# Optimization experiments

Measured on AMD Instinct MI355X. Metric: run time of the kernel, lower is better.

Reference implementation:

```python
import jax, jax.numpy as jnp
import numpy as np

N_SRC = 50000
N_DST = 50000
E = 800000
IN_DIM = 128
OUT_DIM = 64
HEADS = 4
NEG_SLOPE = 0.2  # PyG GATConv default negative_slope
EPS = 1e-16      # PyG softmax denominator epsilon


def setup_inputs() -> dict:
    key = jax.random.key(0)
    ks = jax.random.split(key, 8)
    x_src = jax.random.normal(ks[0], (N_SRC, IN_DIM), dtype=jnp.float32)
    x_dst = jax.random.normal(ks[1], (N_DST, IN_DIM), dtype=jnp.float32)
    src = jax.random.randint(ks[2], (E,), 0, N_SRC, dtype=jnp.int32)
    dst = jax.random.randint(ks[3], (E,), 0, N_DST, dtype=jnp.int32)
    edge_index = jnp.stack([src, dst], axis=0)
    W_src = jax.random.normal(ks[4], (IN_DIM, HEADS * OUT_DIM), dtype=jnp.float32) / np.sqrt(IN_DIM)
    W_dst = jax.random.normal(ks[5], (IN_DIM, HEADS * OUT_DIM), dtype=jnp.float32) / np.sqrt(IN_DIM)
    att_src = jax.random.normal(ks[6], (HEADS, OUT_DIM), dtype=jnp.float32) / np.sqrt(OUT_DIM)
    att_dst = jax.random.normal(ks[7], (HEADS, OUT_DIM), dtype=jnp.float32) / np.sqrt(OUT_DIM)
    bias = jnp.zeros((OUT_DIM,), dtype=jnp.float32)
    return {"x_src": x_src, "x_dst": x_dst, "edge_index": edge_index,
            "W_src": W_src, "W_dst": W_dst, "att_src": att_src,
            "att_dst": att_dst, "bias": bias}


def reference(x_src, x_dst, edge_index, W_src, W_dst, att_src, att_dst, bias):
    # Linear projections -> [N, H, C]
    hs = (x_src @ W_src).reshape(N_SRC, HEADS, OUT_DIM)
    hd = (x_dst @ W_dst).reshape(N_DST, HEADS, OUT_DIM)
    # Per-node attention logits -> [N, H]
    a_s = jnp.einsum('nhc,hc->nh', hs, att_src)
    a_d = jnp.einsum('nhc,hc->nh', hd, att_dst)

    src, dst = edge_index[0], edge_index[1]
    # Per-edge logits [E, H]
    alpha = jax.nn.leaky_relu(a_s[src] + a_d[dst], negative_slope=NEG_SLOPE)
    # Segment softmax over edges sharing the same dst node
    amax = jax.ops.segment_max(alpha, dst, num_segments=N_DST)
    alpha = jnp.exp(alpha - amax[dst])
    denom = jax.ops.segment_sum(alpha, dst, num_segments=N_DST)
    alpha = alpha / (denom[dst] + EPS)
    # (dropout=0 / eval mode: no attention dropout)
    # Message + scatter-add aggregation: out[i] = sum_e alpha_e * hs[src_e]
    msg = hs[src] * alpha[:, :, None]                 # [E, H, C]
    out = jax.ops.segment_sum(msg, dst, num_segments=N_DST)  # [N_dst, H, C]
    # concat=False -> mean over heads, then bias
    return out.mean(axis=1) + bias
```

## Files before the change

kernel.cpp:

```cpp
#include <hip/hip_runtime.h>
#include <hip/hip_bf16.h>

#define N_SRC 50000
#define N_DST 50000
#define NEDGE 800000
#define IND   128
#define HEADS 4
#define CDIM  64
#define HC    256
#define MAXDEG 96
#define NB_ALPHA 12500
#define NB_HIST  3125

typedef _Float16 half8  __attribute__((ext_vector_type(8)));
typedef _Float16 half2t __attribute__((ext_vector_type(2)));
typedef float    f32x4  __attribute__((ext_vector_type(4)));

static __device__ __forceinline__ unsigned int pack2h(float a, float b) {
    union { half2t h; unsigned int u; } v;
    v.h[0] = (_Float16)a; v.h[1] = (_Float16)b;
    return v.u;
}
static __device__ __forceinline__ half2t bits2h(unsigned int u) {
    union { unsigned int u; half2t h; } v; v.u = u; return v.h;
}

__global__ void prep_kernel(const float* __restrict__ Wdst,
                            const float* __restrict__ att_d,
                            float* __restrict__ WdA,
                            const float* __restrict__ Wsrc,
                            _Float16* __restrict__ WhT, int* __restrict__ deg) {
    int b = blockIdx.x, tid = threadIdx.x;
    if (b < 196) {
        int i = b * 256 + tid;
        if (i < N_DST) deg[i] = 0;
    } else if (b < 198) {
        int id = (b - 196) * 256 + tid;
        int k = id >> 2, h = id & 3;
        float acc = 0.f;
        for (int c = 0; c < CDIM; ++c)
            acc += Wdst[k * HC + h * CDIM + c] * att_d[h * CDIM + c];
        WdA[id] = acc;
    } else {
        int idx = (b - 198) * 256 + tid;
        int n = idx >> 7, k = idx & 127;
        WhT[idx] = (_Float16)Wsrc[k * HC + n];
    }
}

__global__ __launch_bounds__(256) void gemm_mfma_kernel(
        const float* __restrict__ x, const _Float16* __restrict__ WhT,
        const float* __restrict__ att_s,
        unsigned short* __restrict__ hsTh, float* __restrict__ a_s) {
    int tid = threadIdx.x;
    int w = tid >> 6, lane = tid & 63;
    int ll = lane & 15, q = lane >> 4;
    int rbase = blockIdx.x * 64 + w * 16;

    int arow = rbase + ll;
    if (arow >= N_SRC) arow = N_SRC - 1;
    const float* xr = x + (size_t)arow * IND + q * 8;
    half8 afrag[4];
    #pragma unroll
    for (int kf = 0; kf < 4; ++kf) {
        float4 u0 = *(const float4*)(xr + kf * 32);
        float4 u1 = *(const float4*)(xr + kf * 32 + 4);
        half8 a;
        a[0] = (_Float16)u0.x; a[1] = (_Float16)u0.y;
        a[2] = (_Float16)u0.z; a[3] = (_Float16)u0.w;
        a[4] = (_Float16)u1.x; a[5] = (_Float16)u1.y;
        a[6] = (_Float16)u1.z; a[7] = (_Float16)u1.w;
        afrag[kf] = a;
    }

    f32x4 acc[16];
    #pragma unroll
    for (int t = 0; t < 16; ++t) acc[t] = (f32x4){0.f, 0.f, 0.f, 0.f};

    #pragma unroll
    for (int t = 0; t < 16; ++t) {
        const _Float16* bp = WhT + (size_t)(t * 16 + ll) * IND + q * 8;
        half8 b0 = *(const half8*)(bp + 0);
        half8 b1 = *(const half8*)(bp + 32);
        half8 b2 = *(const half8*)(bp + 64);
        half8 b3 = *(const half8*)(bp + 96);
        f32x4 c = acc[t];
        c = __builtin_amdgcn_mfma_f32_16x16x32_f16(afrag[0], b0, c, 0, 0, 0);
        c = __builtin_amdgcn_mfma_f32_16x16x32_f16(afrag[1], b1, c, 0, 0, 0);
        c = __builtin_amdgcn_mfma_f32_16x16x32_f16(afrag[2], b2, c, 0, 0, 0);
        c = __builtin_amdgcn_mfma_f32_16x16x32_f16(afrag[3], b3, c, 0, 0, 0);
        acc[t] = c;
    }

    #pragma unroll
    for (int tg = 0; tg < 4; ++tg) {
        #pragma unroll
        for (int r = 0; r < 4; ++r) {
            int n = rbase + q * 4 + r;
            if (n < N_SRC) {
                uint2 v;
                v.x = pack2h(acc[tg     ][r], acc[tg + 4 ][r]);
                v.y = pack2h(acc[tg + 8 ][r], acc[tg + 12][r]);
                *(uint2*)(hsTh + (size_t)n * HC + (tg * 16 + ll) * 4) = v;
            }
        }
    }

    float attv[16];
    #pragma unroll
    for (int t = 0; t < 16; ++t) attv[t] = att_s[t * 16 + ll];
    #pragma unroll
    for (int r = 0; r < 4; ++r) {
        float4 p;
        p.x = acc[0][r]*attv[0]  + acc[1][r]*attv[1]  + acc[2][r]*attv[2]  + acc[3][r]*attv[3];
        p.y = acc[4][r]*attv[4]  + acc[5][r]*attv[5]  + acc[6][r]*attv[6]  + acc[7][r]*attv[7];
        p.z = acc[8][r]*attv[8]  + acc[9][r]*attv[9]  + acc[10][r]*attv[10]+ acc[11][r]*attv[11];
        p.w = acc[12][r]*attv[12]+ acc[13][r]*attv[13]+ acc[14][r]*attv[14]+ acc[15][r]*attv[15];
        #pragma unroll
        for (int off = 1; off < 16; off <<= 1) {
            p.x += __shfl_xor(p.x, off, 64);
            p.y += __shfl_xor(p.y, off, 64);
            p.z += __shfl_xor(p.z, off, 64);
            p.w += __shfl_xor(p.w, off, 64);
        }
        int n = rbase + q * 4 + r;
        if (ll == 0 && n < N_SRC) *(float4*)(a_s + (size_t)n * 4) = p;
    }
}

__global__ __launch_bounds__(256) void mid_kernel(
        const float* __restrict__ x_dst, const float* __restrict__ WdA,
        float* __restrict__ a_d,
        const int* __restrict__ src, const int* __restrict__ dst,
        int* __restrict__ deg, int* __restrict__ col2) {
    int b = blockIdx.x, tid = threadIdx.x;
    if (b < NB_ALPHA) {
        int n    = (b * 256 + tid) >> 6;
        int lane = tid & 63;
        const float* xp = x_dst + (size_t)n * IND;
        const float4* wa = (const float4*)WdA;
        float x0 = xp[lane], x1 = xp[lane + 64];
        float4 wa0 = wa[lane], wa1 = wa[lane + 64];
        float p0 = x0 * wa0.x + x1 * wa1.x;
        float p1 = x0 * wa0.y + x1 * wa1.y;
        float p2 = x0 * wa0.z + x1 * wa1.z;
        float p3 = x0 * wa0.w + x1 * wa1.w;
        for (int off = 32; off >= 1; off >>= 1) {
            p0 += __shfl_xor(p0, off, 64);
            p1 += __shfl_xor(p1, off, 64);
            p2 += __shfl_xor(p2, off, 64);
            p3 += __shfl_xor(p3, off, 64);
        }
        if (lane == 0) {
            a_d[n * 4 + 0] = p0; a_d[n * 4 + 1] = p1;
            a_d[n * 4 + 2] = p2; a_d[n * 4 + 3] = p3;
        }
    } else {
        int e = (b - NB_ALPHA) * 256 + tid;
        if (e < NEDGE) {
            int d = dst[e];
            int r = atomicAdd(&deg[d], 1);
            if (r < MAXDEG) col2[d * MAXDEG + r] = src[e];
        }
    }
}

__global__ __launch_bounds__(256) void aggregate_kernel(
        const int* __restrict__ deg, const int* __restrict__ col2,
        const float4* __restrict__ as4, const float4* __restrict__ ad4,
        const unsigned short* __restrict__ hsTh,
        const float* __restrict__ bias, float* __restrict__ out) {
    __shared__ int   s_off[4][MAXDEG];
    __shared__ uint4 s_pk[4][MAXDEG];
    int tid = threadIdx.x;
    int wv = tid >> 6, lane = tid & 63;
    int i = (blockIdx.x * 256 + tid) >> 6;
    if (i >= N_DST) return;
    int dg = deg[i]; if (dg > MAXDEG) dg = MAXDEG;
    float bv = bias[lane];
    if (dg == 0) { out[i * CDIM + lane] = bv; return; }
    float4 ad = ad4[i];
    const int* crow = col2 + i * MAXDEG;

    float s0 = 0.f, s1 = 0.f, s2 = 0.f, s3 = 0.f;
    for (int e = lane; e < dg; e += 64) {
        int sn = crow[e];
        float4 av = as4[sn];
        float lx = av.x + ad.x; lx = lx > 0.f ? lx : 0.2f * lx;
        float ly = av.y + ad.y; ly = ly > 0.f ? ly : 0.2f * ly;
        float lz = av.z + ad.z; lz = lz > 0.f ? lz : 0.2f * lz;
        float lw = av.w + ad.w; lw = lw > 0.f ? lw : 0.2f * lw;
        float w0 = __expf(lx), w1 = __expf(ly), w2 = __expf(lz), w3 = __expf(lw);
        s0 += w0; s1 += w1; s2 += w2; s3 += w3;
        s_off[wv][e] = sn * HC;
        float4 wf = {w0, w1, w2, w3};
        *(float4*)&s_pk[wv][e] = wf;
    }
    for (int off = 32; off >= 1; off >>= 1) {
        s0 += __shfl_xor(s0, off, 64);
        s1 += __shfl_xor(s1, off, 64);
        s2 += __shfl_xor(s2, off, 64);
        s3 += __shfl_xor(s3, off, 64);
    }
    float i0 = 0.25f / (s0 + 1e-16f);
    float i1 = 0.25f / (s1 + 1e-16f);
    float i2 = 0.25f / (s2 + 1e-16f);
    float i3 = 0.25f / (s3 + 1e-16f);

    for (int e = lane; e < dg; e += 64) {
        float4 wf = *(float4*)&s_pk[wv][e];
        uint4 pk;
        pk.x = (unsigned int)s_off[wv][e];
        pk.y = pack2h(wf.x * i0, wf.y * i1);
        pk.z = pack2h(wf.z * i2, wf.w * i3);
        pk.w = 0;
        s_pk[wv][e] = pk;
    }
    __asm__ volatile("s_waitcnt lgkmcnt(0)" ::: "memory");

    const unsigned short* hb = hsTh + (lane << 2);
    float acc = 0.f;
    int j = 0;
    for (; j + 4 <= dg; j += 4) {
        uint4 p0 = s_pk[wv][j];
        uint4 p1 = s_pk[wv][j + 1];
        uint4 p2 = s_pk[wv][j + 2];
        uint4 p3 = s_pk[wv][j + 3];
        uint2 h0 = *(const uint2*)(hb + p0.x);
        uint2 h1 = *(const uint2*)(hb + p1.x);
        uint2 h2 = *(const uint2*)(hb + p2.x);
        uint2 h3 = *(const uint2*)(hb + p3.x);
        acc = __builtin_amdgcn_fdot2(bits2h(h0.x), bits2h(p0.y), acc, false);
        acc = __builtin_amdgcn_fdot2(bits2h(h0.y), bits2h(p0.z), acc, false);
        acc = __builtin_amdgcn_fdot2(bits2h(h1.x), bits2h(p1.y), acc, false);
        acc = __builtin_amdgcn_fdot2(bits2h(h1.y), bits2h(p1.z), acc, false);
        acc = __builtin_amdgcn_fdot2(bits2h(h2.x), bits2h(p2.y), acc, false);
        acc = __builtin_amdgcn_fdot2(bits2h(h2.y), bits2h(p2.z), acc, false);
        acc = __builtin_amdgcn_fdot2(bits2h(h3.x), bits2h(p3.y), acc, false);
        acc = __builtin_amdgcn_fdot2(bits2h(h3.y), bits2h(p3.z), acc, false);
    }
    for (; j < dg; ++j) {
        uint4 p0 = s_pk[wv][j];
        uint2 h0 = *(const uint2*)(hb + p0.x);
        acc = __builtin_amdgcn_fdot2(bits2h(h0.x), bits2h(p0.y), acc, false);
        acc = __builtin_amdgcn_fdot2(bits2h(h0.y), bits2h(p0.z), acc, false);
    }
    out[i * CDIM + lane] = acc + bv;
}

extern "C" void kernel_launch(void* const* d_in, const int* in_sizes, int n_in,
                              void* d_out, int out_size, void* d_ws, size_t ws_size,
                              hipStream_t stream) {
    const float* x_src   = (const float*)d_in[0];
    const float* x_dst   = (const float*)d_in[1];
    const int*   ei      = (const int*)d_in[2];
    const float* W_src   = (const float*)d_in[3];
    const float* W_dst   = (const float*)d_in[4];
    const float* att_src = (const float*)d_in[5];
    const float* att_dst = (const float*)d_in[6];
    const float* bias    = (const float*)d_in[7];
    float* out = (float*)d_out;

    char* ws = (char*)d_ws;
    unsigned short* hsTh = (unsigned short*)ws; ws += (size_t)N_SRC * HC * 2;
    int*    col2    = (int*)ws;    ws += (size_t)N_DST * MAXDEG * 4;
    float*  a_s     = (float*)ws;  ws += (size_t)N_SRC * 4 * 4;
    float*  a_d     = (float*)ws;  ws += (size_t)N_DST * 4 * 4;
    float*  WdA     = (float*)ws;  ws += 2048;
    _Float16* WhT   = (_Float16*)ws; ws += IND * HC * 2;
    int*    deg     = (int*)ws;    ws += N_DST * 4;

    prep_kernel<<<326, 256, 0, stream>>>(W_dst, att_dst, WdA, W_src, WhT, deg);
    gemm_mfma_kernel<<<(N_SRC + 63) / 64, 256, 0, stream>>>(x_src, WhT, att_src, hsTh, a_s);
    mid_kernel<<<NB_ALPHA + NB_HIST, 256, 0, stream>>>(x_dst, WdA, a_d, ei, ei + NEDGE, deg, col2);
    aggregate_kernel<<<(N_DST + 3) / 4, 256, 0, stream>>>(deg, col2,
                                                          (const float4*)a_s, (const float4*)a_d,
                                                          hsTh, bias, out);
}
```

Before: 256.7 us.

## Partition CSR histogram build by destination range across block groups

Restructures the edge bucketing pass so that 8 groups of blocks each read all edges with vectorized nontemporal loads but only handle destinations in their own range of 6250 nodes. The aim is to localize atomics and col2 writes into a smaller address window per group, which likely maps to distinct XCDs and L2 slices, and to issue the histogram blocks before the a_d projection blocks. The cost is that every edge is read 8 times and most lanes do filtered no-op work.

New measurement: 243.6 us. 1.05x faster.

```diff
diff --git a/kernel.cpp b/kernel.cpp
--- a/kernel.cpp
+++ b/kernel.cpp
@@ -10,11 +10,14 @@
 #define HC    256
 #define MAXDEG 96
 #define NB_ALPHA 12500
-#define NB_HIST  3125
+#define HIST_GPB 256
+#define NB_HIST2 2048
+#define DPG 6250
 
 typedef _Float16 half8  __attribute__((ext_vector_type(8)));
 typedef _Float16 half2t __attribute__((ext_vector_type(2)));
 typedef float    f32x4  __attribute__((ext_vector_type(4)));
+typedef int      i32x4  __attribute__((ext_vector_type(4)));
 
 static __device__ __forceinline__ unsigned int pack2h(float a, float b) {
     union { half2t h; unsigned int u; } v;
@@ -134,8 +137,28 @@
         const int* __restrict__ src, const int* __restrict__ dst,
         int* __restrict__ deg, int* __restrict__ col2) {
     int b = blockIdx.x, tid = threadIdx.x;
-    if (b < NB_ALPHA) {
-        int n    = (b * 256 + tid) >> 6;
+    if (b < NB_HIST2) {
+        int g  = b & 7;
+        int bg = b >> 3;
+        int lo = g * DPG, hi = lo + DPG;
+        #pragma unroll 1
+        for (int it = 0; it < 4; ++it) {
+            int base = ((it * HIST_GPB + bg) << 10) + (tid << 2);
+            if (base >= NEDGE) break;
+            i32x4 dv = __builtin_nontemporal_load((const i32x4*)(dst + base));
+            i32x4 sv = __builtin_nontemporal_load((const i32x4*)(src + base));
+            #pragma unroll
+            for (int j = 0; j < 4; ++j) {
+                int d = dv[j];
+                if (d >= lo && d < hi) {
+                    int r = atomicAdd(&deg[d], 1);
+                    if (r < MAXDEG) col2[d * MAXDEG + r] = sv[j];
+                }
+            }
+        }
+    } else {
+        int rank = b - NB_HIST2;
+        int n    = (rank * 256 + tid) >> 6;
         int lane = tid & 63;
         const float* xp = x_dst + (size_t)n * IND;
         const float4* wa = (const float4*)WdA;
@@ -154,13 +177,6 @@
         if (lane == 0) {
             a_d[n * 4 + 0] = p0; a_d[n * 4 + 1] = p1;
             a_d[n * 4 + 2] = p2; a_d[n * 4 + 3] = p3;
-        }
-    } else {
-        int e = (b - NB_ALPHA) * 256 + tid;
-        if (e < NEDGE) {
-            int d = dst[e];
-            int r = atomicAdd(&deg[d], 1);
-            if (r < MAXDEG) col2[d * MAXDEG + r] = src[e];
         }
     }
 }
@@ -272,7 +288,7 @@
 
     prep_kernel<<<326, 256, 0, stream>>>(W_dst, att_dst, WdA, W_src, WhT, deg);
     gemm_mfma_kernel<<<(N_SRC + 63) / 64, 256, 0, stream>>>(x_src, WhT, att_src, hsTh, a_s);
-    mid_kernel<<<NB_ALPHA + NB_HIST, 256, 0, stream>>>(x_dst, WdA, a_d, ei, ei + NEDGE, deg, col2);
+    mid_kernel<<<NB_HIST2 + NB_ALPHA, 256, 0, stream>>>(x_dst, WdA, a_d, ei, ei + NEDGE, deg, col2);
     aggregate_kernel<<<(N_DST + 3) / 4, 256, 0, stream>>>(deg, col2,
                                                           (const float4*)a_s, (const float4*)a_d,
                                                           hsTh, bias, out);
```

## Two-pass bucketed CSR build: bin edges by destination range before scattering

Applied to the files above, without the earlier changes.

Edge insertion into the per-destination adjacency lists is split into two kernels. The first bins edges into 64 queues keyed by destination group and block parity, using wave-aggregated atomics, and packs the local destination and source into one word. The second kernel has the blocks of each destination group scatter only within that group's 6250 destinations, so the deg atomics and col2 writes stay within a smaller, more cache-resident address window. This costs an extra pass over the edges, an extra launch and queue storage. It also relies on the source id fitting in 17 bits and on no queue exceeding QCAP.

New measurement: 993.2 us. 3.87x slower.

```diff
diff --git a/kernel.cpp b/kernel.cpp
--- a/kernel.cpp
+++ b/kernel.cpp
@@ -9,8 +9,12 @@
 #define CDIM  64
 #define HC    256
 #define MAXDEG 96
-#define NB_ALPHA 12500
-#define NB_HIST  3125
+#define NB_ALPHA  12500
+#define NB_BUCKET 3125
+#define NB_SCAT   2048
+#define DPG  6250
+#define QCAP 16384
+#define NQ   64
 
 typedef _Float16 half8  __attribute__((ext_vector_type(8)));
 typedef _Float16 half2t __attribute__((ext_vector_type(2)));
@@ -29,11 +33,13 @@
                             const float* __restrict__ att_d,
                             float* __restrict__ WdA,
                             const float* __restrict__ Wsrc,
-                            _Float16* __restrict__ WhT, int* __restrict__ deg) {
+                            _Float16* __restrict__ WhT, int* __restrict__ deg,
+                            int* __restrict__ qtail) {
     int b = blockIdx.x, tid = threadIdx.x;
     if (b < 196) {
         int i = b * 256 + tid;
         if (i < N_DST) deg[i] = 0;
+        if (b == 0 && tid < NQ) qtail[tid] = 0;
     } else if (b < 198) {
         int id = (b - 196) * 256 + tid;
         int k = id >> 2, h = id & 3;
@@ -128,14 +134,37 @@
     }
 }
 
-__global__ __launch_bounds__(256) void mid_kernel(
+__global__ __launch_bounds__(256) void mid1_kernel(
         const float* __restrict__ x_dst, const float* __restrict__ WdA,
         float* __restrict__ a_d,
         const int* __restrict__ src, const int* __restrict__ dst,
-        int* __restrict__ deg, int* __restrict__ col2) {
+        unsigned int* __restrict__ q, int* __restrict__ qtail) {
     int b = blockIdx.x, tid = threadIdx.x;
-    if (b < NB_ALPHA) {
-        int n    = (b * 256 + tid) >> 6;
+    if (b < NB_BUCKET) {
+        int e = b * 256 + tid;
+        int d = __builtin_nontemporal_load(dst + e);
+        int s = __builtin_nontemporal_load(src + e);
+        unsigned int g    = (unsigned int)d / DPG;
+        unsigned int dloc = (unsigned int)d - g * DPG;
+        unsigned int v    = (dloc << 17) | (unsigned int)s;
+        int lane = tid & 63;
+        int qi = (int)g * 8 + (b & 7);
+        #pragma unroll
+        for (unsigned int gi = 0; gi < 8; ++gi) {
+            unsigned long long m = __ballot(g == gi);
+            if (g == gi) {
+                int leader = __ffsll(m) - 1;
+                int myoff  = __popcll(m & ((1ull << lane) - 1ull));
+                int base = 0;
+                if (lane == leader) base = atomicAdd(&qtail[qi], __popcll(m));
+                base = __shfl(base, leader, 64);
+                int slot = base + myoff;
+                if (slot < QCAP) q[(size_t)qi * QCAP + slot] = v;
+            }
+        }
+    } else {
+        int rank = b - NB_BUCKET;
+        int n    = (rank * 256 + tid) >> 6;
         int lane = tid & 63;
         const float* xp = x_dst + (size_t)n * IND;
         const float4* wa = (const float4*)WdA;
@@ -155,12 +184,27 @@
             a_d[n * 4 + 0] = p0; a_d[n * 4 + 1] = p1;
             a_d[n * 4 + 2] = p2; a_d[n * 4 + 3] = p3;
         }
-    } else {
-        int e = (b - NB_ALPHA) * 256 + tid;
-        if (e < NEDGE) {
-            int d = dst[e];
+    }
+}
+
+__global__ __launch_bounds__(256) void mid2_kernel(
+        const unsigned int* __restrict__ q, const int* __restrict__ qtail,
+        int* __restrict__ deg, int* __restrict__ col2) {
+    int b = blockIdx.x, tid = threadIdx.x;
+    int g  = b & 7;
+    int bg = b >> 3;
+    int base_d = g * DPG;
+    #pragma unroll 1
+    for (int sq = 0; sq < 8; ++sq) {
+        int qi = g * 8 + sq;
+        int n = qtail[qi]; if (n > QCAP) n = QCAP;
+        const unsigned int* qp = q + (size_t)qi * QCAP;
+        for (int idx = bg * 256 + tid; idx < n; idx += NB_SCAT / 8 * 256) {
+            unsigned int v = qp[idx];
+            int s = (int)(v & 0x1FFFFu);
+            int d = base_d + (int)(v >> 17);
             int r = atomicAdd(&deg[d], 1);
-            if (r < MAXDEG) col2[d * MAXDEG + r] = src[e];
+            if (r < MAXDEG) col2[d * MAXDEG + r] = s;
         }
     }
 }
@@ -264,15 +308,19 @@
     char* ws = (char*)d_ws;
     unsigned short* hsTh = (unsigned short*)ws; ws += (size_t)N_SRC * HC * 2;
     int*    col2    = (int*)ws;    ws += (size_t)N_DST * MAXDEG * 4;
+    unsigned int* q = (unsigned int*)ws; ws += (size_t)NQ * QCAP * 4;
     float*  a_s     = (float*)ws;  ws += (size_t)N_SRC * 4 * 4;
     float*  a_d     = (float*)ws;  ws += (size_t)N_DST * 4 * 4;
     float*  WdA     = (float*)ws;  ws += 2048;
     _Float16* WhT   = (_Float16*)ws; ws += IND * HC * 2;
     int*    deg     = (int*)ws;    ws += N_DST * 4;
-
-    prep_kernel<<<326, 256, 0, stream>>>(W_dst, att_dst, WdA, W_src, WhT, deg);
+    int*    qtail   = (int*)ws;    ws += NQ * 4;
+
+    prep_kernel<<<326, 256, 0, stream>>>(W_dst, att_dst, WdA, W_src, WhT, deg, qtail);
     gemm_mfma_kernel<<<(N_SRC + 63) / 64, 256, 0, stream>>>(x_src, WhT, att_src, hsTh, a_s);
-    mid_kernel<<<NB_ALPHA + NB_HIST, 256, 0, stream>>>(x_dst, WdA, a_d, ei, ei + NEDGE, deg, col2);
+    mid1_kernel<<<NB_BUCKET + NB_ALPHA, 256, 0, stream>>>(x_dst, WdA, a_d,
+                                                          ei, ei + NEDGE, q, qtail);
+    mid2_kernel<<<NB_SCAT, 256, 0, stream>>>(q, qtail, deg, col2);
     aggregate_kernel<<<(N_DST + 3) / 4, 256, 0, stream>>>(deg, col2,
                                                           (const float4*)a_s, (const float4*)a_d,
                                                           hsTh, bias, out);
```
